# Optimization experiments

Hardware: AMD Instinct MI355X
Metric: run time of the kernel (lower is better)

Reference implementation:

```python
import jax, jax.numpy as jnp
import numpy as np

N_NODES = 100000


def _gcn_layer(x, src, dst, W, b, num_nodes):
    # Linear transform first (PyG GCNConv applies Linear before propagate).
    h = x @ W.T  # [N, out]
    # Degree (with self loops already included in src/dst), computed on target.
    ones = jnp.ones(dst.shape[0], dtype=h.dtype)
    deg = jax.ops.segment_sum(ones, dst, num_segments=num_nodes)
    dinv = jnp.where(deg > 0, jax.lax.rsqrt(deg), 0.0)
    norm = dinv[src] * dinv[dst]  # [E]
    msg = h[src] * norm[:, None]  # gather + per-edge scale, [E, out]
    out = jax.ops.segment_sum(msg, dst, num_segments=num_nodes)
    return out + b


def setup_inputs() -> dict:
    key = jax.random.key(0)
    k1, k2, k3, k4, k5, k6 = jax.random.split(key, 6)
    d = 64
    x = jax.random.normal(k1, (N_NODES, d), dtype=jnp.float32)
    edge_index = jax.random.randint(k2, (2, 1600000), 0, N_NODES, dtype=jnp.int64)
    s = 1.0 / np.sqrt(d)
    W1 = jax.random.normal(k3, (d, d), dtype=jnp.float32) * s
    b1 = jax.random.normal(k4, (d,), dtype=jnp.float32) * 0.01
    W2 = jax.random.normal(k5, (d, d), dtype=jnp.float32) * s
    b2 = jax.random.normal(k6, (d,), dtype=jnp.float32) * 0.01
    return {"x": x, "edge_index": edge_index, "W1": W1, "b1": b1, "W2": W2, "b2": b2}


def reference(x, edge_index, W1, b1, W2, b2):
    n = x.shape[0]
    loop = jnp.arange(n, dtype=edge_index.dtype)
    src = jnp.concatenate([edge_index[0], loop])  # add self loops
    dst = jnp.concatenate([edge_index[1], loop])
    h = _gcn_layer(x, src, dst, W1, b1, n)
    out = _gcn_layer(h, src, dst, W2, b2, n)
    return out
```

## Files before the change

kernel.cpp:

```cpp
#include <hip/hip_runtime.h>
#include <hip/hip_fp16.h>


#define D 64
#define NPB 128
#define MAXB 784
#define CHUNK 8192

__global__ __launch_bounds__(256) void hist_kernel(const int* __restrict__ dst,
                                                   int* __restrict__ counts,
                                                   int* __restrict__ cursor,
                                                   int nE, int B) {
    __shared__ int hist[MAXB];
    if (blockIdx.x == 0 && threadIdx.x == 0) *cursor = 0;
    int c = blockIdx.x;
    for (int b = threadIdx.x; b < B; b += 256) hist[b] = 0;
    __syncthreads();
    int e0 = c * CHUNK;
#pragma unroll
    for (int i = 0; i < CHUNK / 256; ++i) {
        int e = e0 + i * 256 + threadIdx.x;
        if (e < nE) atomicAdd(&hist[dst[e] >> 7], 1);
    }
    __syncthreads();
    for (int b = threadIdx.x; b < B; b += 256) counts[c * B + b] = hist[b];
}

__global__ __launch_bounds__(256) void scan_alloc(int* __restrict__ counts,
                                                  int* __restrict__ btot,
                                                  int* __restrict__ bbase,
                                                  int* __restrict__ cursor,
                                                  int B, int C) {
    int b = blockIdx.x * 4 + (threadIdx.x >> 6);
    if (b >= B) return;
    int lane = threadIdx.x & 63;
    int running = 0;
    for (int c0 = 0; c0 < C; c0 += 64) {
        int c = c0 + lane;
        int v = (c < C) ? counts[c * B + b] : 0;
        int x = v;
#pragma unroll
        for (int s = 1; s < 64; s <<= 1) {
            int u = __shfl_up(x, s);
            if (lane >= s) x += u;
        }
        if (c < C) counts[c * B + b] = running + x - v;
        running += __shfl(x, 63);
    }
    if (lane == 0) {
        int base = atomicAdd(cursor, running);
        bbase[b] = base;
        btot[b]  = running;
    }
}

__global__ __launch_bounds__(256) void scatter0_kernel(const int* __restrict__ src,
                                                       const int* __restrict__ dst,
                                                       const int* __restrict__ base,
                                                       const int* __restrict__ bbase,
                                                       int* __restrict__ entries0,
                                                       int nE, int B) {
    __shared__ int cur[MAXB];
    int c = blockIdx.x;
    for (int b = threadIdx.x; b < B; b += 256) cur[b] = base[c * B + b] + bbase[b];
    __syncthreads();
    int e0 = c * CHUNK;
#pragma unroll
    for (int i = 0; i < CHUNK / 256; ++i) {
        int e = e0 + i * 256 + threadIdx.x;
        if (e < nE) {
            int s = src[e], d = dst[e];
            int pos = atomicAdd(&cur[d >> 7], 1);
            entries0[pos] = s | ((d & (NPB - 1)) << 17);
        }
    }
}

__global__ __launch_bounds__(256) void regroup_kernel(const int* __restrict__ entries0,
                                                      const int* __restrict__ bbase,
                                                      const int* __restrict__ btot,
                                                      int* __restrict__ off,
                                                      int* __restrict__ deg,
                                                      float* __restrict__ dinv,
                                                      int* __restrict__ entries1, int N) {
    __shared__ int cnt[NPB];
    __shared__ int scn[NPB];
    __shared__ int cur[NPB];
    int b = blockIdx.x;
    int t = threadIdx.x;
    if (t < NPB) cnt[t] = 0;
    __syncthreads();
    int s0 = bbase[b], s1 = s0 + btot[b];
    for (int p = s0 + t; p < s1; p += 256)
        atomicAdd(&cnt[(entries0[p] >> 17) & (NPB - 1)], 1);
    __syncthreads();
    if (t < NPB) scn[t] = cnt[t];
    __syncthreads();
    for (int s = 1; s < NPB; s <<= 1) {
        int u = 0;
        if (t < NPB && t >= s) u = scn[t - s];
        __syncthreads();
        if (t < NPB) scn[t] += u;
        __syncthreads();
    }
    if (t < NPB) {
        int node = b * NPB + t;
        int c = cnt[t];
        int o = s0 + scn[t] - c;
        cur[t] = o;
        if (node < N) {
            off[node]  = o;
            deg[node]  = c;
            dinv[node] = rsqrtf((float)c + 1.0f);
        }
    }
    __syncthreads();
    for (int p = s0 + t; p < s1; p += 256) {
        int e = entries0[p];
        int pos = atomicAdd(&cur[(e >> 17) & (NPB - 1)], 1);
        entries1[pos] = e & 0x1FFFF;
    }
}

template <typename OutT>
__global__ __launch_bounds__(256) void aggregate3(const int* __restrict__ csr,
                                                  const int* __restrict__ off,
                                                  const int* __restrict__ deg,
                                                  const float* __restrict__ dinv,
                                                  const __half* __restrict__ H,
                                                  const float* __restrict__ bias,
                                                  OutT* __restrict__ out, int N) {
    int node = blockIdx.x * 4 + (threadIdx.x >> 6);
    if (node >= N) return;
    int lane = threadIdx.x & 63;
    int p2 = lane & 31;
    int h  = lane >> 5;
    const __half2* H2 = (const __half2*)H;
    float dd = dinv[node];
    float2 acc = make_float2(0.0f, 0.0f);
    int beg = off[node];
    int end = beg + deg[node];
    int p = beg;
    for (; p + 16 <= end; p += 16) {
        int s[8];
#pragma unroll
        for (int i = 0; i < 8; ++i) s[i] = csr[p + 2 * i + h];
        __half2 g[8];
        float dv[8];
#pragma unroll
        for (int i = 0; i < 8; ++i) {
            g[i]  = H2[(size_t)s[i] * 32 + p2];
            dv[i] = dinv[s[i]];
        }
#pragma unroll
        for (int i = 0; i < 8; ++i) {
            float2 f = __half22float2(g[i]);
            float c = dv[i] * dd;
            acc.x += f.x * c; acc.y += f.y * c;
        }
    }
    for (; p + 8 <= end; p += 8) {
        int s0v = csr[p + 0 + h], s1v = csr[p + 2 + h];
        int s2v = csr[p + 4 + h], s3v = csr[p + 6 + h];
        __half2 g0 = H2[(size_t)s0v * 32 + p2];
        __half2 g1 = H2[(size_t)s1v * 32 + p2];
        __half2 g2 = H2[(size_t)s2v * 32 + p2];
        __half2 g3 = H2[(size_t)s3v * 32 + p2];
        float c0 = dinv[s0v] * dd, c1 = dinv[s1v] * dd;
        float c2 = dinv[s2v] * dd, c3 = dinv[s3v] * dd;
        float2 f0 = __half22float2(g0), f1 = __half22float2(g1);
        float2 f2 = __half22float2(g2), f3 = __half22float2(g3);
        acc.x += f0.x * c0; acc.y += f0.y * c0;
        acc.x += f1.x * c1; acc.y += f1.y * c1;
        acc.x += f2.x * c2; acc.y += f2.y * c2;
        acc.x += f3.x * c3; acc.y += f3.y * c3;
    }
    for (; p + 2 <= end; p += 2) {
        int s0v = csr[p + h];
        __half2 g0 = H2[(size_t)s0v * 32 + p2];
        float c0 = dinv[s0v] * dd;
        float2 f0 = __half22float2(g0);
        acc.x += f0.x * c0; acc.y += f0.y * c0;
    }
    if (p < end && h == 0) {
        int s0v = csr[p];
        __half2 g0 = H2[(size_t)s0v * 32 + p2];
        float c0 = dinv[s0v] * dd;
        float2 f0 = __half22float2(g0);
        acc.x += f0.x * c0; acc.y += f0.y * c0;
    }
    acc.x += __shfl_xor(acc.x, 32);
    acc.y += __shfl_xor(acc.y, 32);
    if (h == 0) {
        float s = dd * dd;
        float2 hs = __half22float2(H2[(size_t)node * 32 + p2]);
        float2 bv = ((const float2*)bias)[p2];
        float2 o;
        o.x = acc.x + bv.x + hs.x * s;
        o.y = acc.y + bv.y + hs.y * s;
        if constexpr (sizeof(OutT) == 2) {
            ((__half2*)(out + (size_t)node * D))[p2] = __float22half2_rn(o);
        } else {
            ((float2*)(out + (size_t)node * D))[p2] = o;
        }
    }
}

template <typename InT>
__global__ __launch_bounds__(256) void gemm_xwt_h(const InT* __restrict__ X,
                                                  const float* __restrict__ W,
                                                  __half* __restrict__ H, int N) {
    __shared__ float xt[64 * 68];
    __shared__ float wt[64 * 68];
    const int t = threadIdx.x;
    const int i0 = blockIdx.x * 64;
#pragma unroll
    for (int r = 0; r < 16; ++r) {
        int idx = r * 256 + t;
        int j = idx >> 6, k = idx & 63;
        wt[k * 68 + j] = W[idx];
    }
#pragma unroll
    for (int r = 0; r < 16; ++r) {
        int idx = r * 256 + t;
        int i = idx >> 6, k = idx & 63;
        float v = 0.0f;
        if (i0 + i < N) {
            if constexpr (sizeof(InT) == 2)
                v = __half2float(((const __half*)X)[(size_t)(i0 + i) * D + k]);
            else
                v = ((const float*)X)[(size_t)(i0 + i) * D + k];
        }
        xt[k * 68 + i] = v;
    }
    __syncthreads();
    const int tn = (t & 15) * 4;
    const int tc = (t >> 4) * 4;
    float acc[4][4] = {};
#pragma unroll 8
    for (int k = 0; k < 64; ++k) {
        const float4 xa = *(const float4*)(xt + k * 68 + tn);
        const float4 wb = *(const float4*)(wt + k * 68 + tc);
        acc[0][0] += xa.x * wb.x; acc[0][1] += xa.x * wb.y; acc[0][2] += xa.x * wb.z; acc[0][3] += xa.x * wb.w;
        acc[1][0] += xa.y * wb.x; acc[1][1] += xa.y * wb.y; acc[1][2] += xa.y * wb.z; acc[1][3] += xa.y * wb.w;
        acc[2][0] += xa.z * wb.x; acc[2][1] += xa.z * wb.y; acc[2][2] += xa.z * wb.z; acc[2][3] += xa.z * wb.w;
        acc[3][0] += xa.w * wb.x; acc[3][1] += xa.w * wb.y; acc[3][2] += xa.w * wb.z; acc[3][3] += xa.w * wb.w;
    }
#pragma unroll
    for (int a = 0; a < 4; ++a) {
        int i = i0 + tn + a;
        if (i < N) {
            union { __half2 h2[2]; uint2 u2; } pk;
            pk.h2[0].x = __float2half_rn(acc[a][0]);
            pk.h2[0].y = __float2half_rn(acc[a][1]);
            pk.h2[1].x = __float2half_rn(acc[a][2]);
            pk.h2[1].y = __float2half_rn(acc[a][3]);
            *(uint2*)(&H[(size_t)i * D + tc]) = pk.u2;
        }
    }
}

__global__ __launch_bounds__(256) void deg_kernel(const int* __restrict__ dst,
                                                  int* __restrict__ deg, int nE) {
    int e = blockIdx.x * 256 + threadIdx.x;
    if (e < nE) atomicAdd(&deg[dst[e]], 1);
}

__global__ __launch_bounds__(256) void dinv_kernel(const int* __restrict__ deg,
                                                   float* __restrict__ dinv, int N) {
    int i = blockIdx.x * 256 + threadIdx.x;
    if (i < N) dinv[i] = rsqrtf((float)deg[i] + 1.0f);
}

__global__ __launch_bounds__(256) void gemm_xwt(const float* __restrict__ X,
                                                const float* __restrict__ W,
                                                float* __restrict__ H, int N) {
    __shared__ float xt[64 * 68];
    __shared__ float wt[64 * 68];
    const int t = threadIdx.x;
    const int i0 = blockIdx.x * 64;
#pragma unroll
    for (int r = 0; r < 16; ++r) {
        int idx = r * 256 + t;
        int j = idx >> 6, k = idx & 63;
        wt[k * 68 + j] = W[idx];
    }
#pragma unroll
    for (int r = 0; r < 16; ++r) {
        int idx = r * 256 + t;
        int i = idx >> 6, k = idx & 63;
        float v = 0.0f;
        if (i0 + i < N) v = X[(size_t)(i0 + i) * D + k];
        xt[k * 68 + i] = v;
    }
    __syncthreads();
    const int tn = (t & 15) * 4;
    const int tc = (t >> 4) * 4;
    float acc[4][4] = {};
#pragma unroll 8
    for (int k = 0; k < 64; ++k) {
        const float4 xa = *(const float4*)(xt + k * 68 + tn);
        const float4 wb = *(const float4*)(wt + k * 68 + tc);
        acc[0][0] += xa.x * wb.x; acc[0][1] += xa.x * wb.y; acc[0][2] += xa.x * wb.z; acc[0][3] += xa.x * wb.w;
        acc[1][0] += xa.y * wb.x; acc[1][1] += xa.y * wb.y; acc[1][2] += xa.y * wb.z; acc[1][3] += xa.y * wb.w;
        acc[2][0] += xa.z * wb.x; acc[2][1] += xa.z * wb.y; acc[2][2] += xa.z * wb.z; acc[2][3] += xa.z * wb.w;
        acc[3][0] += xa.w * wb.x; acc[3][1] += xa.w * wb.y; acc[3][2] += xa.w * wb.z; acc[3][3] += xa.w * wb.w;
    }
#pragma unroll
    for (int a = 0; a < 4; ++a) {
        int i = i0 + tn + a;
        if (i < N) {
            float4 o = make_float4(acc[a][0], acc[a][1], acc[a][2], acc[a][3]);
            *(float4*)(H + (size_t)i * D + tc) = o;
        }
    }
}

__global__ __launch_bounds__(256) void init_out(const float* __restrict__ H,
                                                const float* __restrict__ dinv,
                                                const float* __restrict__ b,
                                                float* __restrict__ out, int N) {
    int idx4 = blockIdx.x * 256 + threadIdx.x;
    if (idx4 >= N * 16) return;
    int i = idx4 >> 4;
    int jc = idx4 & 15;
    float di = dinv[i];
    float s = di * di;
    float4 h4 = ((const float4*)H)[idx4];
    float4 b4 = ((const float4*)b)[jc];
    ((float4*)out)[idx4] = make_float4(b4.x + h4.x * s, b4.y + h4.y * s,
                                       b4.z + h4.z * s, b4.w + h4.w * s);
}

__global__ __launch_bounds__(256) void edge_scatter(const int* __restrict__ src,
                                                    const int* __restrict__ dst,
                                                    const float* __restrict__ dinv,
                                                    const float* __restrict__ H,
                                                    float* __restrict__ out, int nE) {
    int tid = blockIdx.x * 256 + threadIdx.x;
    int e = tid >> 4;
    if (e >= nE) return;
    int l = tid & 15;
    int s = src[e];
    int d = dst[e];
    float c = dinv[s] * dinv[d];
    float4 v = ((const float4*)H)[s * 16 + l];
    float* o = out + (size_t)d * D + l * 4;
    unsafeAtomicAdd(o + 0, v.x * c);
    unsafeAtomicAdd(o + 1, v.y * c);
    unsafeAtomicAdd(o + 2, v.z * c);
    unsafeAtomicAdd(o + 3, v.w * c);
}

static inline size_t align_up(size_t v, size_t a) { return (v + a - 1) & ~(a - 1); }

extern "C" void kernel_launch(void* const* d_in, const int* in_sizes, int n_in,
                              void* d_out, int out_size, void* d_ws, size_t ws_size,
                              hipStream_t stream) {
    const float* x  = (const float*)d_in[0];
    const int*   ei = (const int*)d_in[1];
    const float* W1 = (const float*)d_in[2];
    const float* b1 = (const float*)d_in[3];
    const float* W2 = (const float*)d_in[4];
    const float* b2 = (const float*)d_in[5];
    float* out = (float*)d_out;

    const int N  = in_sizes[0] / D;
    const int nE = in_sizes[1] / 2;
    const int* srcp = ei;
    const int* dstv = ei + nE;

    const int B = (N + NPB - 1) / NPB;
    const int C = (nE + CHUNK - 1) / CHUNK;

    char* base_p = (char*)d_ws;
    size_t o = 0;
    int* counts = (int*)(base_p + o);  o = align_up(o + (size_t)C * B * 4, 256);
    int* btot   = (int*)(base_p + o);  o = align_up(o + (size_t)B * 4, 256);
    int* bbase  = (int*)(base_p + o);  o = align_up(o + (size_t)B * 4, 256);
    int* cursor = (int*)(base_p + o);  o = align_up(o + 4, 256);
    int* off    = (int*)(base_p + o);  o = align_up(o + (size_t)N * 4, 256);
    int* deg    = (int*)(base_p + o);  o = align_up(o + (size_t)N * 4, 256);
    float* dinv = (float*)(base_p + o); o = align_up(o + (size_t)N * 4, 256);
    int* entries1 = (int*)(base_p + o); o = align_up(o + (size_t)nE * 4, 256);
    size_t r2 = (size_t)nE * 4 > (size_t)N * D * 2 ? (size_t)nE * 4 : (size_t)N * D * 2;
    int* entries0 = (int*)(base_p + o);
    __half* Hh    = (__half*)(base_p + o);
    o = align_up(o + r2, 256);
    size_t need_base = o;
    __half* A1h = (__half*)(base_p + o);
    size_t need_full = o + align_up((size_t)N * D * 2, 256);

    int gb_n = (N + 255) / 256;
    int gb_g = (N + 63) / 64;
    int gb_e = (nE + 255) / 256;

    if (ws_size >= need_base && B <= MAXB) {
        hist_kernel<<<C, 256, 0, stream>>>(dstv, counts, cursor, nE, B);
        scan_alloc<<<(B + 3) / 4, 256, 0, stream>>>(counts, btot, bbase, cursor, B, C);
        scatter0_kernel<<<C, 256, 0, stream>>>(srcp, dstv, counts, bbase, entries0, nE, B);
        regroup_kernel<<<B, 256, 0, stream>>>(entries0, bbase, btot, off, deg, dinv, entries1, N);

        int gb_a = (N + 3) / 4;
        gemm_xwt_h<float><<<gb_g, 256, 0, stream>>>(x, W1, Hh, N);
        if (ws_size >= need_full) {
            aggregate3<__half><<<gb_a, 256, 0, stream>>>(entries1, off, deg, dinv, Hh, b1, A1h, N);
            gemm_xwt_h<__half><<<gb_g, 256, 0, stream>>>(A1h, W2, Hh, N);
        } else {
            aggregate3<float><<<gb_a, 256, 0, stream>>>(entries1, off, deg, dinv, Hh, b1, out, N);
            gemm_xwt_h<float><<<gb_g, 256, 0, stream>>>(out, W2, Hh, N);
        }
        aggregate3<float><<<gb_a, 256, 0, stream>>>(entries1, off, deg, dinv, Hh, b2, out, N);
    } else {
        size_t fo = 0;
        int* fdeg    = (int*)(base_p + fo);  fo = align_up(fo + (size_t)N * 4, 256);
        float* fdinv = (float*)(base_p + fo); fo = align_up(fo + (size_t)N * 4, 256);
        float* bufA  = (float*)(base_p + fo);
        hipMemsetAsync(fdeg, 0, (size_t)N * 4, stream);
        deg_kernel<<<gb_e, 256, 0, stream>>>(dstv, fdeg, nE);
        dinv_kernel<<<gb_n, 256, 0, stream>>>(fdeg, fdinv, N);
        int gb_i = (N * 16 + 255) / 256;
        int gb_e16 = (int)(((long long)nE * 16 + 255) / 256);
        gemm_xwt<<<gb_g, 256, 0, stream>>>(x, W1, bufA, N);
        init_out<<<gb_i, 256, 0, stream>>>(bufA, fdinv, b1, out, N);
        edge_scatter<<<gb_e16, 256, 0, stream>>>(srcp, dstv, fdinv, bufA, out, nE);
        gemm_xwt<<<gb_g, 256, 0, stream>>>(out, W2, bufA, N);
        init_out<<<gb_i, 256, 0, stream>>>(bufA, fdinv, b2, out, N);
        edge_scatter<<<gb_e16, 256, 0, stream>>>(srcp, dstv, fdinv, bufA, out, nE);
    }
}
```

Baseline: 282.2 us.

## Fuse first GEMM into histogram launch and second GEMM into aggregation

The first X·W1ᵀ GEMM now runs as extra blocks of the histogram kernel, so it overlaps with edge bucketing instead of running as its own launch after CSR construction. The first-layer aggregation is fused with the W2 transform: each block aggregates four nodes into shared memory and multiplies by W2 there, which removes the fp16 intermediate round trip and one GEMM launch. Each agg_gemm block reloads W2 into shared memory and does a small per-node matvec, which adds per-block overhead. The 16-wide unrolled gather loop is dropped from the aggregation, and the workspace layout gives H its own buffer.

```diff
diff --git a/kernel.cpp b/kernel.cpp
--- a/kernel.cpp
+++ b/kernel.cpp
@@ -7,23 +7,73 @@
 #define MAXB 784
 #define CHUNK 8192
 
-__global__ __launch_bounds__(256) void hist_kernel(const int* __restrict__ dst,
-                                                   int* __restrict__ counts,
-                                                   int* __restrict__ cursor,
-                                                   int nE, int B) {
-    __shared__ int hist[MAXB];
-    if (blockIdx.x == 0 && threadIdx.x == 0) *cursor = 0;
-    int c = blockIdx.x;
-    for (int b = threadIdx.x; b < B; b += 256) hist[b] = 0;
-    __syncthreads();
-    int e0 = c * CHUNK;
-#pragma unroll
-    for (int i = 0; i < CHUNK / 256; ++i) {
-        int e = e0 + i * 256 + threadIdx.x;
-        if (e < nE) atomicAdd(&hist[dst[e] >> 7], 1);
-    }
-    __syncthreads();
-    for (int b = threadIdx.x; b < B; b += 256) counts[c * B + b] = hist[b];
+__global__ __launch_bounds__(256) void hist_gemm1(const int* __restrict__ dst,
+                                                  int* __restrict__ counts,
+                                                  int* __restrict__ cursor,
+                                                  const float* __restrict__ X,
+                                                  const float* __restrict__ W1,
+                                                  __half* __restrict__ H,
+                                                  int nE, int B, int C, int N) {
+    __shared__ __align__(16) char smem[34816];
+    const int t = threadIdx.x;
+    if ((int)blockIdx.x < C) {
+        int* hist = (int*)smem;
+        if (blockIdx.x == 0 && t == 0) *cursor = 0;
+        int c = blockIdx.x;
+        for (int b = t; b < B; b += 256) hist[b] = 0;
+        __syncthreads();
+        int e0 = c * CHUNK;
+#pragma unroll
+        for (int i = 0; i < CHUNK / 256; ++i) {
+            int e = e0 + i * 256 + t;
+            if (e < nE) atomicAdd(&hist[dst[e] >> 7], 1);
+        }
+        __syncthreads();
+        for (int b = t; b < B; b += 256) counts[c * B + b] = hist[b];
+    } else {
+        float* xt = (float*)smem;
+        float* wt = xt + 64 * 68;
+        const int i0 = ((int)blockIdx.x - C) * 64;
+#pragma unroll
+        for (int r = 0; r < 16; ++r) {
+            int idx = r * 256 + t;
+            int j = idx >> 6, k = idx & 63;
+            wt[k * 68 + j] = W1[idx];
+        }
+#pragma unroll
+        for (int r = 0; r < 16; ++r) {
+            int idx = r * 256 + t;
+            int i = idx >> 6, k = idx & 63;
+            float v = 0.0f;
+            if (i0 + i < N) v = X[(size_t)(i0 + i) * D + k];
+            xt[k * 68 + i] = v;
+        }
+        __syncthreads();
+        const int tn = (t & 15) * 4;
+        const int tc = (t >> 4) * 4;
+        float acc[4][4] = {};
+#pragma unroll 8
+        for (int k = 0; k < 64; ++k) {
+            const float4 xa = *(const float4*)(xt + k * 68 + tn);
+            const float4 wb = *(const float4*)(wt + k * 68 + tc);
+            acc[0][0] += xa.x * wb.x; acc[0][1] += xa.x * wb.y; acc[0][2] += xa.x * wb.z; acc[0][3] += xa.x * wb.w;
+            acc[1][0] += xa.y * wb.x; acc[1][1] += xa.y * wb.y; acc[1][2] += xa.y * wb.z; acc[1][3] += xa.y * wb.w;
+            acc[2][0] += xa.z * wb.x; acc[2][1] += xa.z * wb.y; acc[2][2] += xa.z * wb.z; acc[2][3] += xa.z * wb.w;
+            acc[3][0] += xa.w * wb.x; acc[3][1] += xa.w * wb.y; acc[3][2] += xa.w * wb.z; acc[3][3] += xa.w * wb.w;
+        }
+#pragma unroll
+        for (int a = 0; a < 4; ++a) {
+            int i = i0 + tn + a;
+            if (i < N) {
+                union { __half2 h2[2]; uint2 u2; } pk;
+                pk.h2[0].x = __float2half_rn(acc[a][0]);
+                pk.h2[0].y = __float2half_rn(acc[a][1]);
+                pk.h2[1].x = __float2half_rn(acc[a][2]);
+                pk.h2[1].y = __float2half_rn(acc[a][3]);
+                *(uint2*)(&H[(size_t)i * D + tc]) = pk.u2;
+            }
+        }
+    }
 }
 
 __global__ __launch_bounds__(256) void scan_alloc(int* __restrict__ counts,
@@ -122,14 +172,97 @@
     }
 }
 
-template <typename OutT>
+__global__ __launch_bounds__(256) void agg_gemm(const int* __restrict__ csr,
+                                                const int* __restrict__ off,
+                                                const int* __restrict__ deg,
+                                                const float* __restrict__ dinv,
+                                                const __half* __restrict__ H,
+                                                const float* __restrict__ b1,
+                                                const float* __restrict__ W2,
+                                                __half* __restrict__ H2out, int N) {
+    __shared__ float w2t[64 * 65];
+    __shared__ float rows[4][64];
+    const int t = threadIdx.x;
+#pragma unroll
+    for (int r = 0; r < 16; ++r) {
+        int idx = r * 256 + t;
+        int j = idx >> 6, k = idx & 63;
+        w2t[k * 65 + j] = W2[idx];
+    }
+    __syncthreads();
+
+    int node = blockIdx.x * 4 + (t >> 6);
+    int lane = t & 63;
+    int w = t >> 6;
+    int p2 = lane & 31;
+    int h  = lane >> 5;
+    const __half2* H2 = (const __half2*)H;
+
+    if (node < N) {
+        float dd = dinv[node];
+        float2 acc = make_float2(0.0f, 0.0f);
+        int beg = off[node];
+        int end = beg + deg[node];
+        int p = beg;
+        for (; p + 8 <= end; p += 8) {
+            int s0v = csr[p + 0 + h], s1v = csr[p + 2 + h];
+            int s2v = csr[p + 4 + h], s3v = csr[p + 6 + h];
+            __half2 g0 = H2[(size_t)s0v * 32 + p2];
+            __half2 g1 = H2[(size_t)s1v * 32 + p2];
+            __half2 g2 = H2[(size_t)s2v * 32 + p2];
+            __half2 g3 = H2[(size_t)s3v * 32 + p2];
+            float c0 = dinv[s0v] * dd, c1 = dinv[s1v] * dd;
+            float c2 = dinv[s2v] * dd, c3 = dinv[s3v] * dd;
+            float2 f0 = __half22float2(g0), f1 = __half22float2(g1);
+            float2 f2 = __half22float2(g2), f3 = __half22float2(g3);
+            acc.x += f0.x * c0; acc.y += f0.y * c0;
+            acc.x += f1.x * c1; acc.y += f1.y * c1;
+            acc.x += f2.x * c2; acc.y += f2.y * c2;
+            acc.x += f3.x * c3; acc.y += f3.y * c3;
+        }
+        for (; p + 2 <= end; p += 2) {
+            int s0v = csr[p + h];
+            __half2 g0 = H2[(size_t)s0v * 32 + p2];
+            float c0 = dinv[s0v] * dd;
+            float2 f0 = __half22float2(g0);
+            acc.x += f0.x * c0; acc.y += f0.y * c0;
+        }
+        if (p < end && h == 0) {
+            int s0v = csr[p];
+            __half2 g0 = H2[(size_t)s0v * 32 + p2];
+            float c0 = dinv[s0v] * dd;
+            float2 f0 = __half22float2(g0);
+            acc.x += f0.x * c0; acc.y += f0.y * c0;
+        }
+        acc.x += __shfl_xor(acc.x, 32);
+        acc.y += __shfl_xor(acc.y, 32);
+        if (h == 0) {
+            float s = dd * dd;
+            float2 hs = __half22float2(H2[(size_t)node * 32 + p2]);
+            float2 bv = ((const float2*)b1)[p2];
+            rows[w][2 * p2]     = acc.x + bv.x + hs.x * s;
+            rows[w][2 * p2 + 1] = acc.y + bv.y + hs.y * s;
+        }
+    }
+    __syncthreads();
+
+    if (node < N) {
+        float o = 0.0f;
+        const float* rw = rows[w];
+#pragma unroll 8
+        for (int k = 0; k < 64; ++k)
+            o += rw[k] * w2t[k * 65 + lane];
+        H2out[(size_t)node * D + lane] = __float2half_rn(o);
+    }
+}
+
 __global__ __launch_bounds__(256) void aggregate3(const int* __restrict__ csr,
                                                   const int* __restrict__ off,
                                                   const int* __restrict__ deg,
                                                   const float* __restrict__ dinv,
                                                   const __half* __restrict__ H,
                                                   const float* __restrict__ bias,
-                                                  OutT* __restrict__ out, int N) {
+                                                  float* __restrict__ out, int N) {
     int node = blockIdx.x * 4 + (threadIdx.x >> 6);
     if (node >= N) return;
     int lane = threadIdx.x & 63;
@@ -141,24 +274,6 @@
     int beg = off[node];
     int end = beg + deg[node];
     int p = beg;
-    for (; p + 16 <= end; p += 16) {
-        int s[8];
-#pragma unroll
-        for (int i = 0; i < 8; ++i) s[i] = csr[p + 2 * i + h];
-        __half2 g[8];
-        float dv[8];
-#pragma unroll
-        for (int i = 0; i < 8; ++i) {
-            g[i]  = H2[(size_t)s[i] * 32 + p2];
-            dv[i] = dinv[s[i]];
-        }
-#pragma unroll
-        for (int i = 0; i < 8; ++i) {
-            float2 f = __half22float2(g[i]);
-            float c = dv[i] * dd;
-            acc.x += f.x * c; acc.y += f.y * c;
-        }
-    }
     for (; p + 8 <= end; p += 8) {
         int s0v = csr[p + 0 + h], s1v = csr[p + 2 + h];
         int s2v = csr[p + 4 + h], s3v = csr[p + 6 + h];
@@ -198,12 +313,27 @@
         float2 o;
         o.x = acc.x + bv.x + hs.x * s;
         o.y = acc.y + bv.y + hs.y * s;
-        if constexpr (sizeof(OutT) == 2) {
-            ((__half2*)(out + (size_t)node * D))[p2] = __float22half2_rn(o);
-        } else {
-            ((float2*)(out + (size_t)node * D))[p2] = o;
-        }
-    }
+        ((float2*)(out + (size_t)node * D))[p2] = o;
+    }
+}
+
+__global__ __launch_bounds__(256) void hist_kernel(const int* __restrict__ dst,
+                                                   int* __restrict__ counts,
+                                                   int* __restrict__ cursor,
+                                                   int nE, int B) {
+    __shared__ int hist[MAXB];
+    if (blockIdx.x == 0 && threadIdx.x == 0) *cursor = 0;
+    int c = blockIdx.x;
+    for (int b = threadIdx.x; b < B; b += 256) hist[b] = 0;
+    __syncthreads();
+    int e0 = c * CHUNK;
+#pragma unroll
+    for (int i = 0; i < CHUNK / 256; ++i) {
+        int e = e0 + i * 256 + threadIdx.x;
+        if (e < nE) atomicAdd(&hist[dst[e] >> 7], 1);
+    }
+    __syncthreads();
+    for (int b = threadIdx.x; b < B; b += 256) counts[c * B + b] = hist[b];
 }
 
 template <typename InT>
@@ -383,34 +513,38 @@
     int* deg    = (int*)(base_p + o);  o = align_up(o + (size_t)N * 4, 256);
     float* dinv = (float*)(base_p + o); o = align_up(o + (size_t)N * 4, 256);
     int* entries1 = (int*)(base_p + o); o = align_up(o + (size_t)nE * 4, 256);
+    __half* Hh  = (__half*)(base_p + o); o = align_up(o + (size_t)N * D * 2, 256);
     size_t r2 = (size_t)nE * 4 > (size_t)N * D * 2 ? (size_t)nE * 4 : (size_t)N * D * 2;
     int* entries0 = (int*)(base_p + o);
-    __half* Hh    = (__half*)(base_p + o);
+    __half* Hh2   = (__half*)(base_p + o);
     o = align_up(o + r2, 256);
-    size_t need_base = o;
-    __half* A1h = (__half*)(base_p + o);
-    size_t need_full = o + align_up((size_t)N * D * 2, 256);
+    size_t need_fused = o;
+    size_t need_mid = need_fused - align_up((size_t)N * D * 2, 256);
 
     int gb_n = (N + 255) / 256;
     int gb_g = (N + 63) / 64;
     int gb_e = (nE + 255) / 256;
-
-    if (ws_size >= need_base && B <= MAXB) {
-        hist_kernel<<<C, 256, 0, stream>>>(dstv, counts, cursor, nE, B);
+    int gb_a = (N + 3) / 4;
+
+    if (ws_size >= need_fused && B <= MAXB) {
+        hist_gemm1<<<C + gb_g, 256, 0, stream>>>(dstv, counts, cursor,
+                                                 x, W1, Hh, nE, B, C, N);
         scan_alloc<<<(B + 3) / 4, 256, 0, stream>>>(counts, btot, bbase, cursor, B, C);
         scatter0_kernel<<<C, 256, 0, stream>>>(srcp, dstv, counts, bbase, entries0, nE, B);
         regroup_kernel<<<B, 256, 0, stream>>>(entries0, bbase, btot, off, deg, dinv, entries1, N);
-
-        int gb_a = (N + 3) / 4;
-        gemm_xwt_h<float><<<gb_g, 256, 0, stream>>>(x, W1, Hh, N);
-        if (ws_size >= need_full) {
-            aggregate3<__half><<<gb_a, 256, 0, stream>>>(entries1, off, deg, dinv, Hh, b1, A1h, N);
-            gemm_xwt_h<__half><<<gb_g, 256, 0, stream>>>(A1h, W2, Hh, N);
-        } else {
-            aggregate3<float><<<gb_a, 256, 0, stream>>>(entries1, off, deg, dinv, Hh, b1, out, N);
-            gemm_xwt_h<float><<<gb_g, 256, 0, stream>>>(out, W2, Hh, N);
-        }
-        aggregate3<float><<<gb_a, 256, 0, stream>>>(entries1, off, deg, dinv, Hh, b2, out, N);
+        agg_gemm<<<gb_a, 256, 0, stream>>>(entries1, off, deg, dinv, Hh, b1, W2, Hh2, N);
+        aggregate3<<<gb_a, 256, 0, stream>>>(entries1, off, deg, dinv, Hh2, b2, out, N);
+    } else if (ws_size >= need_mid && B <= MAXB) {
+        int* e0m = (int*)Hh;
+        __half* Hm = Hh;
+        hist_kernel<<<C, 256, 0, stream>>>(dstv, counts, cursor, nE, B);
+        scan_alloc<<<(B + 3) / 4, 256, 0, stream>>>(counts, btot, bbase, cursor, B, C);
+        scatter0_kernel<<<C, 256, 0, stream>>>(srcp, dstv, counts, bbase, e0m, nE, B);
+        regroup_kernel<<<B, 256, 0, stream>>>(e0m, bbase, btot, off, deg, dinv, entries1, N);
+        gemm_xwt_h<float><<<gb_g, 256, 0, stream>>>(x, W1, Hm, N);
+        aggregate3<<<gb_a, 256, 0, stream>>>(entries1, off, deg, dinv, Hm, b1, out, N);
+        gemm_xwt_h<float><<<gb_g, 256, 0, stream>>>(out, W2, Hm, N);
+        aggregate3<<<gb_a, 256, 0, stream>>>(entries1, off, deg, dinv, Hm, b2, out, N);
     } else {
         size_t fo = 0;
         int* fdeg    = (int*)(base_p + fo);  fo = align_up(fo + (size_t)N * 4, 256);
```

Result: slower. 292.3 us (+3.6%).
